# Optimization experiments

Measured on AMD Instinct MI355X. Metric: run time of the kernel, lower is better.

## Reference

```python
import jax, jax.numpy as jnp
from jax import lax
import numpy as np

# (mult_l0, mult_l1, mult_l2) per layer, from CNN.__init__
FEATS = [(5, 0, 0), (10, 3, 0), (10, 3, 1), (16, 8, 1), (16, 8, 1), (16, 8, 1), (1, 0, 0)]
STRIDES = [2, 1, 1, 1, 1, 1]
RELUS = [True, True, True, True, True, False]
SIZE, NRAD, PAD = 7, 3, 3  # SE3Convolution(size=7, n_radial=3, padding=3)


def ch(r):
    return r[0] + 3 * r[1] + 5 * r[2]


def radial_basis():
    # precomputed fixed radial shell basis on the 7^3 kernel grid (stand-in for
    # e3nn's precomputed spherical-harmonic x radial kernel basis)
    r = np.arange(SIZE) - SIZE // 2
    X, Y, Z = np.meshgrid(r, r, r, indexing='ij')
    dist = np.sqrt(X ** 2 + Y ** 2 + Z ** 2)
    centers = np.linspace(0.0, SIZE // 2, NRAD)
    sigma = (SIZE // 2) / (NRAD - 1)
    b = np.exp(-((dist[None] - centers[:, None, None, None]) ** 2) / (2.0 * sigma ** 2))
    return jnp.asarray(b, jnp.float32)  # [NRAD, 7, 7, 7]


def setup_inputs() -> dict:
    key = jax.random.key(0)
    ks = jax.random.split(key, 20)
    inp = {"x": jax.random.normal(ks[0], (2, 5, 32, 32, 32), jnp.float32)}
    for i in range(6):
        cin = ch(FEATS[i]) + 9 * FEATS[i][1]  # after TensorProduct concat
        cout = ch(FEATS[i + 1])
        inp[f"w{i}"] = jax.random.normal(ks[1 + i], (cout, cin, NRAD), jnp.float32) / np.sqrt(cin * SIZE ** 3)
    for i in range(5):
        inp[f"b{i}"] = jax.random.normal(ks[7 + i], (FEATS[i + 1][0],), jnp.float32) * 0.1
    inp["lin_w"] = jax.random.normal(ks[13], (1, 5), jnp.float32)
    inp["lin_b"] = jax.random.normal(ks[14], (1,), jnp.float32)
    inp["alpha"] = jnp.ones((1,), jnp.float32)
    return inp


def _block(x, w, bias, rep_in, rep_out, stride, relu, basis):
    m1, m3, m5 = rep_in
    B = x.shape[0]
    if m3 > 0:
        # TensorProduct on the l=1 fields: self outer product -> 3x3 (9-dim) fields
        sp = x.shape[2:]
        v = x[:, m1:m1 + 3 * m3].reshape(B, m3, 3, *sp)
        t = jnp.einsum('bmixyz,bmjxyz->bmijxyz', v, v).reshape(B, m3 * 9, *sp)
        x = jnp.concatenate([x, t], axis=1)
    # SE3Convolution: learned mixing of precomputed kernel basis, then conv3d
    k = jnp.einsum('oir,rxyz->oixyz', w, basis)  # [Cout, Cin, 7,7,7]
    x = lax.conv_general_dilated(x, k, (stride,) * 3, [(PAD, PAD)] * 3,
                                 dimension_numbers=('NCDHW', 'OIDHW', 'NCDHW'))
    if relu:
        n1, n3, n5 = rep_out
        sp = x.shape[2:]
        # SE3BatchNorm: per-field norm over batch + spatial (per multiplicity channel)
        parts, off = [], 0
        for m, d in ((n1, 1), (n3, 3), (n5, 5)):
            if m == 0:
                continue
            f = x[:, off:off + m * d].reshape(B, m, d, *sp)
            norm2 = jnp.mean(jnp.sum(f * f, axis=2), axis=(0, 2, 3, 4))  # [m]
            f = f / jnp.sqrt(norm2 + 1e-5)[None, :, None, None, None, None]
            parts.append(f.reshape(B, m * d, *sp))
            off += m * d
        x = jnp.concatenate(parts, axis=1)
        # BiasRelu: bias + relu on scalar (l=0) fields only, higher-l pass through
        s = jax.nn.relu(x[:, :n1] + bias[None, :, None, None, None])
        x = jnp.concatenate([s, x[:, n1:]], axis=1)
    return x


def reference(x, w0, w1, w2, w3, w4, w5, b0, b1, b2, b3, b4, lin_w, lin_b, alpha):
    basis = radial_basis()
    ws = [w0, w1, w2, w3, w4, w5]
    bs = [b0, b1, b2, b3, b4, None]
    inp = x
    for i in range(6):
        x = _block(x, ws[i], bs[i], FEATS[i], FEATS[i + 1], STRIDES[i], RELUS[i], basis)
    B = x.shape[0]
    out = x.reshape(B, x.shape[1], -1).mean(-1) * alpha * 0.1  # [B, 1]
    y = inp.reshape(B, 5, -1).sum(-1) @ lin_w.T + lin_b  # [B, 1]
    return out + y
```

## Files before the change

### kernel.cpp

```cpp
#include <hip/hip_runtime.h>
#include <math.h>

static constexpr int OFF_BAS = 0;
static constexpr int OFF_W   = 1280;
static constexpr int OFF_ACC = 37504;
static constexpr int OFF_XA  = 37888;
static constexpr int OFF_XB  = OFF_XA + 761856;
static constexpr int OFF_U   = OFF_XB + 761856;
static constexpr int OFF_Y   = OFF_U + 1105920;

static constexpr int WOFF0 = OFF_W + 0;
static constexpr int WOFF1 = OFF_W + 384;
static constexpr int WOFF2 = OFF_W + 3264;
static constexpr int WOFF3 = OFF_W + 9248;
static constexpr int WOFF4 = OFF_W + 22304;
static constexpr int WOFF5 = OFF_W + 35360;

__device__ __forceinline__ float wred(float s) {
  #pragma unroll
  for (int o = 32; o > 0; o >>= 1) s += __shfl_xor(s, o, 64);
  return s;
}

__global__ __launch_bounds__(128) void prep_kernel(
    const float* __restrict__ w0, const float* __restrict__ w1,
    const float* __restrict__ w2, const float* __restrict__ w3,
    const float* __restrict__ w4, const float* __restrict__ w5,
    float* __restrict__ ws) {
  const int blk = blockIdx.x;
  const int tid = threadIdx.x;
  if (blk == 0) {
    for (int i = tid; i < 1176; i += 128) {
      int tx = i & 7;
      int r  = (i >> 3) % 3;
      int ty = (i / 24) % 7;
      int tz = i / 168;
      float val = 0.f;
      if (tx < 7) {
        double dx = tx - 3, dy = ty - 3, dz = tz - 3;
        double dist = sqrt(dx * dx + dy * dy + dz * dz);
        double d = dist - 1.5 * (double)r;
        val = (float)exp(-(d * d) / 4.5);
      }
      ws[OFF_BAS + i] = val;
    }
    return;
  }
  const int row = blk - 1;
  const int rs[6]    = {0, 24, 96, 232, 368, 504};
  const int kk[6]    = {15, 37, 42, 93, 93, 93};
  const int k4[6]    = {16, 40, 44, 96, 96, 96};
  const int coutt[6] = {19, 24, 45, 45, 45, 1};
  const int cinf[6]  = {5, 46, 51, 117, 117, 117};
  const int chin_[6] = {5, 19, 24, 45, 45, 45};
  const int woff[6]  = {WOFF0, WOFF1, WOFF2, WOFF3, WOFF4, WOFF5};
  const float* wptr[6] = {w0, w1, w2, w3, w4, w5};
  int l = 0;
  while (l < 5 && row >= rs[l + 1]) ++l;
  const int m = row - rs[l];
  const int K = kk[l], K4 = k4[l];
  const float* w = wptr[l];
  float* Wo = ws + woff[l] + m * K4;
  if (l == 0) {
    for (int k = tid; k < 16; k += 128) {
      float v = 0.f;
      if (m < 19 && k < 15) { int c = k / 3, r = k % 3; v = w[(m * 5 + c) * 3 + r]; }
      Wo[k] = v;
    }
    return;
  }
  const int o = m / 3, r = m % 3;
  const int cout = coutt[l];
  const int cf = cinf[l], ch = chin_[l];
  const int itab[6] = {0, 0, 0, 1, 1, 2};
  const int jtab[6] = {0, 1, 2, 1, 2, 2};
  for (int k = tid; k < K4; k += 128) {
    float v = 0.f;
    if (o < cout && k < K) {
      if (k < ch) {
        v = w[(o * cf + k) * 3 + r];
      } else {
        int cc = k - ch;
        int mm = cc / 6, uu = cc % 6;
        int i = itab[uu], j = jtab[uu];
        v = w[(o * cf + ch + mm * 9 + i * 3 + j) * 3 + r];
        if (i != j) v += w[(o * cf + ch + mm * 9 + j * 3 + i) * 3 + r];
      }
    }
    Wo[k] = v;
  }
}

__global__ __launch_bounds__(256) void insum_kernel(const float* __restrict__ x,
                                                    float* __restrict__ insum) {
  const int g = blockIdx.x * 256 + threadIdx.x;
  float4 v = ((const float4*)x)[g];
  float s = v.x + v.y + v.z + v.w;
  s = wred(s);
  if ((threadIdx.x & 63) == 0) atomicAdd(&insum[g >> 13], s);
}

__global__ __launch_bounds__(256) void dw0_kernel(const float* __restrict__ x,
                                                  const float* __restrict__ basg,
                                                  float* __restrict__ z0) {
  const int g = blockIdx.x * 256 + threadIdx.x;
  const int p = g & 4095;
  const int c = (g >> 12) % 5;
  const int b = g / (5 * 4096);
  const int X = p & 15, Y = (p >> 4) & 15, Z = p >> 8;
  const float* xp = x + (((size_t)(b * 5 + c)) << 15);
  float a0 = 0.f, a1 = 0.f, a2 = 0.f;
  for (int tz = 0; tz < 7; ++tz) {
    const int iz = 2 * Z + tz - 3;
    if ((unsigned)iz >= 32u) continue;
    for (int ty = 0; ty < 7; ++ty) {
      const int iy = 2 * Y + ty - 3;
      if ((unsigned)iy >= 32u) continue;
      const float* bb = &basg[(tz * 7 + ty) * 24];
      const float* row = xp + (iz << 10) + (iy << 5);
      #pragma unroll
      for (int tx = 0; tx < 7; ++tx) {
        const int ix = 2 * X + tx - 3;
        float v = ((unsigned)ix < 32u) ? row[ix] : 0.f;
        a0 = fmaf(bb[tx], v, a0);
        a1 = fmaf(bb[8 + tx], v, a1);
        a2 = fmaf(bb[16 + tx], v, a2);
      }
    }
  }
  const size_t base = (((size_t)(b * 15 + c * 3)) << 12) + p;
  z0[base] = a0;
  z0[base + 4096] = a1;
  z0[base + 8192] = a2;
}

template <int K>
__global__ __launch_bounds__(256) void gemm_kernel(
    const float* __restrict__ in, const float* __restrict__ W,
    float* __restrict__ out, int Mreal, float* __restrict__ chsum) {
  constexpr int K4 = (K + 3) & ~3;
  __shared__ float Wl[8 * K4];
  const int b = blockIdx.z;
  const int m0 = blockIdx.y * 8;
  const int p0 = blockIdx.x * 1024 + threadIdx.x * 4;
  for (int i = threadIdx.x; i < 8 * K4; i += 256) Wl[i] = W[m0 * K4 + i];
  __syncthreads();
  const float* ip = in + (((size_t)b * K) << 12) + p0;
  float4 acc[8];
  #pragma unroll
  for (int j = 0; j < 8; ++j) acc[j] = make_float4(0.f, 0.f, 0.f, 0.f);
  int k = 0;
  for (; k + 4 <= K; k += 4) {
    const float4 v0 = *(const float4*)&ip[(size_t)(k + 0) << 12];
    const float4 v1 = *(const float4*)&ip[(size_t)(k + 1) << 12];
    const float4 v2 = *(const float4*)&ip[(size_t)(k + 2) << 12];
    const float4 v3 = *(const float4*)&ip[(size_t)(k + 3) << 12];
    #pragma unroll
    for (int j = 0; j < 8; ++j) {
      const float4 wv = *(const float4*)&Wl[j * K4 + k];
      acc[j].x = fmaf(wv.x, v0.x, acc[j].x); acc[j].y = fmaf(wv.x, v0.y, acc[j].y);
      acc[j].z = fmaf(wv.x, v0.z, acc[j].z); acc[j].w = fmaf(wv.x, v0.w, acc[j].w);
      acc[j].x = fmaf(wv.y, v1.x, acc[j].x); acc[j].y = fmaf(wv.y, v1.y, acc[j].y);
      acc[j].z = fmaf(wv.y, v1.z, acc[j].z); acc[j].w = fmaf(wv.y, v1.w, acc[j].w);
      acc[j].x = fmaf(wv.z, v2.x, acc[j].x); acc[j].y = fmaf(wv.z, v2.y, acc[j].y);
      acc[j].z = fmaf(wv.z, v2.z, acc[j].z); acc[j].w = fmaf(wv.z, v2.w, acc[j].w);
      acc[j].x = fmaf(wv.w, v3.x, acc[j].x); acc[j].y = fmaf(wv.w, v3.y, acc[j].y);
      acc[j].z = fmaf(wv.w, v3.z, acc[j].z); acc[j].w = fmaf(wv.w, v3.w, acc[j].w);
    }
  }
  for (; k < K; ++k) {
    const float4 v = *(const float4*)&ip[(size_t)k << 12];
    #pragma unroll
    for (int j = 0; j < 8; ++j) {
      const float w = Wl[j * K4 + k];
      acc[j].x = fmaf(w, v.x, acc[j].x); acc[j].y = fmaf(w, v.y, acc[j].y);
      acc[j].z = fmaf(w, v.z, acc[j].z); acc[j].w = fmaf(w, v.w, acc[j].w);
    }
  }
  #pragma unroll
  for (int j = 0; j < 8; ++j) {
    const int m = m0 + j;
    if (m < Mreal) *(float4*)&out[(((size_t)(b * Mreal + m)) << 12) + p0] = acc[j];
  }
  if (chsum) {
    #pragma unroll
    for (int j = 0; j < 8; ++j) {
      float s = acc[j].x * acc[j].x + acc[j].y * acc[j].y +
                acc[j].z * acc[j].z + acc[j].w * acc[j].w;
      s = wred(s);
      if ((threadIdx.x & 63) == 0) atomicAdd(&chsum[m0 + j], s);
    }
  }
}

__global__ __launch_bounds__(256) void dwB_kernel(
    const float* __restrict__ u, const float* __restrict__ basg,
    float* __restrict__ y, float* __restrict__ chsum, int cout) {
  __shared__ float lin[15840];
  const int b = blockIdx.y;
  const int o = blockIdx.x >> 2;
  const int zs = blockIdx.x & 3;
  const int tid = threadIdx.x;
  const int z0 = zs * 4;
  const float* ubase = u + (((size_t)(b * 3 * cout + o * 3)) << 12);
  for (int i = tid; i < 15840; i += 256) {
    const int dx = i % 24;
    int t = i / 24;
    const int dy = t % 22;
    t /= 22;
    const int dz = t % 10;
    const int ch = t / 10;
    const int gz = z0 + dz - 3, gy = dy - 3, gx = dx - 4;
    float v = 0.f;
    if ((unsigned)gz < 16u && (unsigned)gy < 16u && (unsigned)gx < 16u)
      v = ubase[(ch << 12) + (gz << 8) + (gy << 4) + gx];
    lin[i] = v;
  }
  __syncthreads();
  const int bx = tid & 3, yy = (tid >> 2) & 15, zz = tid >> 6;
  float acc[4] = {0.f, 0.f, 0.f, 0.f};
  #pragma unroll 1
  for (int tz = 0; tz < 7; ++tz) {
    #pragma unroll 1
    for (int ty = 0; ty < 7; ++ty) {
      const int rb = ((zz + tz) * 22 + (yy + ty)) * 24 + bx * 4;
      float4 a0 = *(const float4*)&lin[rb];
      float4 a1 = *(const float4*)&lin[rb + 4];
      float4 a2 = *(const float4*)&lin[rb + 8];
      float4 b0 = *(const float4*)&lin[rb + 5280];
      float4 b1 = *(const float4*)&lin[rb + 5284];
      float4 b2 = *(const float4*)&lin[rb + 5288];
      float4 c0 = *(const float4*)&lin[rb + 10560];
      float4 c1 = *(const float4*)&lin[rb + 10564];
      float4 c2 = *(const float4*)&lin[rb + 10568];
      const float* bb = &basg[(tz * 7 + ty) * 24];
      const float va[12] = {a0.x,a0.y,a0.z,a0.w,a1.x,a1.y,a1.z,a1.w,a2.x,a2.y,a2.z,a2.w};
      const float vb[12] = {b0.x,b0.y,b0.z,b0.w,b1.x,b1.y,b1.z,b1.w,b2.x,b2.y,b2.z,b2.w};
      const float vc[12] = {c0.x,c0.y,c0.z,c0.w,c1.x,c1.y,c1.z,c1.w,c2.x,c2.y,c2.z,c2.w};
      #pragma unroll
      for (int tx = 0; tx < 7; ++tx) {
        const float w0 = bb[tx], w1 = bb[8 + tx], w2 = bb[16 + tx];
        #pragma unroll
        for (int i2 = 0; i2 < 4; ++i2) {
          acc[i2] = fmaf(w0, va[i2 + tx + 1], acc[i2]);
          acc[i2] = fmaf(w1, vb[i2 + tx + 1], acc[i2]);
          acc[i2] = fmaf(w2, vc[i2 + tx + 1], acc[i2]);
        }
      }
    }
  }
  const int p = ((z0 + zz) << 8) + (yy << 4) + bx * 4;
  float4 outv = {acc[0], acc[1], acc[2], acc[3]};
  *(float4*)&y[(((size_t)(b * cout + o)) << 12) + p] = outv;
  if (chsum) {
    float s = acc[0]*acc[0] + acc[1]*acc[1] + acc[2]*acc[2] + acc[3]*acc[3];
    s = wred(s);
    if ((tid & 63) == 0) atomicAdd(&chsum[o], s);
  }
}

template <int COUT, int N1, int N3>
__global__ __launch_bounds__(64) void post_kernel(
    const float* __restrict__ y, const float* __restrict__ chsum,
    const float* __restrict__ bias, float* __restrict__ xout) {
  constexpr int N5 = (COUT - N1 - 3 * N3) / 5;
  constexpr int CO = COUT + 6 * N3;
  const int b = blockIdx.y;
  const int p = blockIdx.x * 64 + threadIdx.x;
  const float* yp = y + (((size_t)b * COUT) << 12) + p;
  float* xp = xout + (((size_t)b * CO) << 12) + p;
  const float inv = 1.f / 8192.f;
  float vals[COUT];
  #pragma unroll
  for (int c = 0; c < N1; ++c) {
    const float f = 1.f / sqrtf(chsum[c] * inv + 1e-5f);
    const float v = yp[(size_t)c << 12] * f + bias[c];
    vals[c] = v > 0.f ? v : 0.f;
  }
  #pragma unroll
  for (int m = 0; m < N3; ++m) {
    const int c0 = N1 + 3 * m;
    const float f = 1.f / sqrtf((chsum[c0] + chsum[c0 + 1] + chsum[c0 + 2]) * inv + 1e-5f);
    vals[c0]     = yp[(size_t)c0 << 12] * f;
    vals[c0 + 1] = yp[(size_t)(c0 + 1) << 12] * f;
    vals[c0 + 2] = yp[(size_t)(c0 + 2) << 12] * f;
  }
  #pragma unroll
  for (int m = 0; m < N5; ++m) {
    const int c0 = N1 + 3 * N3 + 5 * m;
    const float s5 = chsum[c0] + chsum[c0+1] + chsum[c0+2] + chsum[c0+3] + chsum[c0+4];
    const float f = 1.f / sqrtf(s5 * inv + 1e-5f);
    #pragma unroll
    for (int d = 0; d < 5; ++d) vals[c0 + d] = yp[(size_t)(c0 + d) << 12] * f;
  }
  #pragma unroll
  for (int c = 0; c < COUT; ++c) xp[(size_t)c << 12] = vals[c];
  #pragma unroll
  for (int m = 0; m < N3; ++m) {
    const float v0 = vals[N1 + 3*m], v1 = vals[N1 + 3*m + 1], v2 = vals[N1 + 3*m + 2];
    const float t[6] = {v0*v0, v0*v1, v0*v2, v1*v1, v1*v2, v2*v2};
    #pragma unroll
    for (int uu = 0; uu < 6; ++uu) xp[(size_t)(COUT + m * 6 + uu) << 12] = t[uu];
  }
}

__global__ __launch_bounds__(256) void final_kernel(
    const float* __restrict__ y5, const float* __restrict__ acc,
    const float* __restrict__ lin_w, const float* __restrict__ lin_b,
    const float* __restrict__ alpha, float* __restrict__ out) {
  const int b = blockIdx.x;
  const int tid = threadIdx.x;
  float s = 0.f;
  for (int i = tid; i < 4096; i += 256) s += y5[(b << 12) + i];
  s = wred(s);
  __shared__ float ls[4];
  if ((tid & 63) == 0) ls[tid >> 6] = s;
  __syncthreads();
  if (tid == 0) {
    const float t = ls[0] + ls[1] + ls[2] + ls[3];
    float res = t * (1.f / 4096.f) * alpha[0] * 0.1f;
    const float* insum = acc + 240;
    for (int c = 0; c < 5; ++c) res += insum[b * 5 + c] * lin_w[c];
    res += lin_b[0];
    out[b] = res;
  }
}

extern "C" void kernel_launch(void* const* d_in, const int* in_sizes, int n_in,
                              void* d_out, int out_size, void* d_ws, size_t ws_size,
                              hipStream_t stream) {
  const float* x  = (const float*)d_in[0];
  const float* w0 = (const float*)d_in[1];
  const float* w1 = (const float*)d_in[2];
  const float* w2 = (const float*)d_in[3];
  const float* w3 = (const float*)d_in[4];
  const float* w4 = (const float*)d_in[5];
  const float* w5 = (const float*)d_in[6];
  const float* b0 = (const float*)d_in[7];
  const float* b1 = (const float*)d_in[8];
  const float* b2 = (const float*)d_in[9];
  const float* b3 = (const float*)d_in[10];
  const float* b4 = (const float*)d_in[11];
  const float* lw = (const float*)d_in[12];
  const float* lb = (const float*)d_in[13];
  const float* al = (const float*)d_in[14];
  float* out = (float*)d_out;
  float* ws = (float*)d_ws;

  float* bas = ws + OFF_BAS;
  float* acc = ws + OFF_ACC;
  float* XA = ws + OFF_XA;
  float* XB = ws + OFF_XB;
  float* U  = ws + OFF_U;
  float* Y  = ws + OFF_Y;

  hipMemsetAsync(acc, 0, 256 * sizeof(float), stream);
  hipLaunchKernelGGL(prep_kernel, dim3(513), dim3(128), 0, stream, w0, w1, w2, w3, w4, w5, ws);
  hipLaunchKernelGGL(insum_kernel, dim3(320), dim3(256), 0, stream, x, acc + 240);

  hipLaunchKernelGGL(dw0_kernel, dim3(160), dim3(256), 0, stream, x, bas, U);
  hipLaunchKernelGGL(gemm_kernel<15>, dim3(4, 3, 2), dim3(256), 0, stream,
                     U, ws + WOFF0, Y, 19, acc);
  hipLaunchKernelGGL((post_kernel<19, 10, 3>), dim3(64, 2), dim3(64), 0, stream, Y, acc, b0, XA);

  hipLaunchKernelGGL(gemm_kernel<37>, dim3(4, 9, 2), dim3(256), 0, stream,
                     XA, ws + WOFF1, U, 72, (float*)nullptr);
  hipLaunchKernelGGL(dwB_kernel, dim3(96, 2), dim3(256), 0, stream, U, bas, Y, acc + 48, 24);
  hipLaunchKernelGGL((post_kernel<24, 10, 3>), dim3(64, 2), dim3(64), 0, stream, Y, acc + 48, b1, XB);

  hipLaunchKernelGGL(gemm_kernel<42>, dim3(4, 17, 2), dim3(256), 0, stream,
                     XB, ws + WOFF2, U, 135, (float*)nullptr);
  hipLaunchKernelGGL(dwB_kernel, dim3(180, 2), dim3(256), 0, stream, U, bas, Y, acc + 96, 45);
  hipLaunchKernelGGL((post_kernel<45, 16, 8>), dim3(64, 2), dim3(64), 0, stream, Y, acc + 96, b2, XA);

  hipLaunchKernelGGL(gemm_kernel<93>, dim3(4, 17, 2), dim3(256), 0, stream,
                     XA, ws + WOFF3, U, 135, (float*)nullptr);
  hipLaunchKernelGGL(dwB_kernel, dim3(180, 2), dim3(256), 0, stream, U, bas, Y, acc + 144, 45);
  hipLaunchKernelGGL((post_kernel<45, 16, 8>), dim3(64, 2), dim3(64), 0, stream, Y, acc + 144, b3, XB);

  hipLaunchKernelGGL(gemm_kernel<93>, dim3(4, 17, 2), dim3(256), 0, stream,
                     XB, ws + WOFF4, U, 135, (float*)nullptr);
  hipLaunchKernelGGL(dwB_kernel, dim3(180, 2), dim3(256), 0, stream, U, bas, Y, acc + 192, 45);
  hipLaunchKernelGGL((post_kernel<45, 16, 8>), dim3(64, 2), dim3(64), 0, stream, Y, acc + 192, b4, XA);

  hipLaunchKernelGGL(gemm_kernel<93>, dim3(4, 1, 2), dim3(256), 0, stream,
                     XA, ws + WOFF5, U, 3, (float*)nullptr);
  hipLaunchKernelGGL(dwB_kernel, dim3(4, 2), dim3(256), 0, stream, U, bas, Y, (float*)nullptr, 1);

  hipLaunchKernelGGL(final_kernel, dim3(2), dim3(256), 0, stream, Y, acc, lw, lb, al, out);
}
```

Before: 530.0 us.

## Split depthwise conv tiles in y, use float4 swizzled LDS staging

The depthwise 7^3 conv kernel now tiles output as 4z x 8y x 16x per block with 128 threads instead of 4z x 16y x 16x with 256 threads, doubling the grid. The halo is loaded with float4 global reads into 32-float rows with an XOR swizzle on odd rows to cut LDS bank conflicts. The smaller per-block LDS footprint should let more blocks share a CU, improving occupancy and load balance. The cost is a larger y-halo overhead (14 staged rows for 8 outputs instead of 22 for 16) and extra index arithmetic.

```diff
diff --git a/kernel.cpp b/kernel.cpp
--- a/kernel.cpp
+++ b/kernel.cpp
@@ -193,46 +193,53 @@
   }
 }
 
-__global__ __launch_bounds__(256) void dwB_kernel(
+__global__ __launch_bounds__(128) void dwB_kernel(
     const float* __restrict__ u, const float* __restrict__ basg,
     float* __restrict__ y, float* __restrict__ chsum, int cout) {
-  __shared__ float lin[15840];
+  __shared__ float lin[13440];
   const int b = blockIdx.y;
-  const int o = blockIdx.x >> 2;
-  const int zs = blockIdx.x & 3;
+  const int o = blockIdx.x >> 3;
+  const int rem = blockIdx.x & 7;
+  const int zs = rem >> 1, yh = rem & 1;
+  const int z0 = zs * 4, y0 = yh * 8;
   const int tid = threadIdx.x;
-  const int z0 = zs * 4;
   const float* ubase = u + (((size_t)(b * 3 * cout + o * 3)) << 12);
-  for (int i = tid; i < 15840; i += 256) {
-    const int dx = i % 24;
-    int t = i / 24;
-    const int dy = t % 22;
-    t /= 22;
-    const int dz = t % 10;
-    const int ch = t / 10;
-    const int gz = z0 + dz - 3, gy = dy - 3, gx = dx - 4;
-    float v = 0.f;
-    if ((unsigned)gz < 16u && (unsigned)gy < 16u && (unsigned)gx < 16u)
-      v = ubase[(ch << 12) + (gz << 8) + (gy << 4) + gx];
-    lin[i] = v;
+  for (int i = tid; i < 3360; i += 128) {
+    const int g = i & 7;
+    const int row = i >> 3;
+    const int ch = row / 140;
+    const int rr = row - ch * 140;
+    const int dz = rr / 14;
+    const int dy = rr - dz * 14;
+    const int gz = z0 + dz - 3, gy = y0 + dy - 3;
+    float4 v = make_float4(0.f, 0.f, 0.f, 0.f);
+    if (g >= 1 && g <= 4 && (unsigned)gz < 16u && (unsigned)gy < 16u)
+      v = *(const float4*)&ubase[(ch << 12) + (gz << 8) + (gy << 4) + ((g - 1) << 2)];
+    const int sw = (dy & 1) << 2;
+    *(float4*)&lin[row * 32 + ((g ^ sw) << 2)] = v;
   }
   __syncthreads();
-  const int bx = tid & 3, yy = (tid >> 2) & 15, zz = tid >> 6;
+  const int bx = tid & 3, yy = (tid >> 2) & 7, zz = tid >> 5;
   float acc[4] = {0.f, 0.f, 0.f, 0.f};
   #pragma unroll 1
   for (int tz = 0; tz < 7; ++tz) {
     #pragma unroll 1
     for (int ty = 0; ty < 7; ++ty) {
-      const int rb = ((zz + tz) * 22 + (yy + ty)) * 24 + bx * 4;
-      float4 a0 = *(const float4*)&lin[rb];
-      float4 a1 = *(const float4*)&lin[rb + 4];
-      float4 a2 = *(const float4*)&lin[rb + 8];
-      float4 b0 = *(const float4*)&lin[rb + 5280];
-      float4 b1 = *(const float4*)&lin[rb + 5284];
-      float4 b2 = *(const float4*)&lin[rb + 5288];
-      float4 c0 = *(const float4*)&lin[rb + 10560];
-      float4 c1 = *(const float4*)&lin[rb + 10564];
-      float4 c2 = *(const float4*)&lin[rb + 10568];
+      const int dy = yy + ty;
+      const int sw = (dy & 1) << 2;
+      const int r0 = ((zz + tz) * 14 + dy) * 32;
+      const int i0 = r0 + (((bx + 0) ^ sw) << 2);
+      const int i1 = r0 + (((bx + 1) ^ sw) << 2);
+      const int i2w = r0 + (((bx + 2) ^ sw) << 2);
+      float4 a0 = *(const float4*)&lin[i0];
+      float4 a1 = *(const float4*)&lin[i1];
+      float4 a2 = *(const float4*)&lin[i2w];
+      float4 b0 = *(const float4*)&lin[i0 + 4480];
+      float4 b1 = *(const float4*)&lin[i1 + 4480];
+      float4 b2 = *(const float4*)&lin[i2w + 4480];
+      float4 c0 = *(const float4*)&lin[i0 + 8960];
+      float4 c1 = *(const float4*)&lin[i1 + 8960];
+      float4 c2 = *(const float4*)&lin[i2w + 8960];
       const float* bb = &basg[(tz * 7 + ty) * 24];
       const float va[12] = {a0.x,a0.y,a0.z,a0.w,a1.x,a1.y,a1.z,a1.w,a2.x,a2.y,a2.z,a2.w};
       const float vb[12] = {b0.x,b0.y,b0.z,b0.w,b1.x,b1.y,b1.z,b1.w,b2.x,b2.y,b2.z,b2.w};
@@ -249,7 +256,7 @@
       }
     }
   }
-  const int p = ((z0 + zz) << 8) + (yy << 4) + bx * 4;
+  const int p = ((z0 + zz) << 8) + ((y0 + yy) << 4) + bx * 4;
   float4 outv = {acc[0], acc[1], acc[2], acc[3]};
   *(float4*)&y[(((size_t)(b * cout + o)) << 12) + p] = outv;
   if (chsum) {
@@ -365,27 +372,27 @@
 
   hipLaunchKernelGGL(gemm_kernel<37>, dim3(4, 9, 2), dim3(256), 0, stream,
                      XA, ws + WOFF1, U, 72, (float*)nullptr);
-  hipLaunchKernelGGL(dwB_kernel, dim3(96, 2), dim3(256), 0, stream, U, bas, Y, acc + 48, 24);
+  hipLaunchKernelGGL(dwB_kernel, dim3(192, 2), dim3(128), 0, stream, U, bas, Y, acc + 48, 24);
   hipLaunchKernelGGL((post_kernel<24, 10, 3>), dim3(64, 2), dim3(64), 0, stream, Y, acc + 48, b1, XB);
 
   hipLaunchKernelGGL(gemm_kernel<42>, dim3(4, 17, 2), dim3(256), 0, stream,
                      XB, ws + WOFF2, U, 135, (float*)nullptr);
-  hipLaunchKernelGGL(dwB_kernel, dim3(180, 2), dim3(256), 0, stream, U, bas, Y, acc + 96, 45);
+  hipLaunchKernelGGL(dwB_kernel, dim3(360, 2), dim3(128), 0, stream, U, bas, Y, acc + 96, 45);
   hipLaunchKernelGGL((post_kernel<45, 16, 8>), dim3(64, 2), dim3(64), 0, stream, Y, acc + 96, b2, XA);
 
   hipLaunchKernelGGL(gemm_kernel<93>, dim3(4, 17, 2), dim3(256), 0, stream,
                      XA, ws + WOFF3, U, 135, (float*)nullptr);
-  hipLaunchKernelGGL(dwB_kernel, dim3(180, 2), dim3(256), 0, stream, U, bas, Y, acc + 144, 45);
+  hipLaunchKernelGGL(dwB_kernel, dim3(360, 2), dim3(128), 0, stream, U, bas, Y, acc + 144, 45);
   hipLaunchKernelGGL((post_kernel<45, 16, 8>), dim3(64, 2), dim3(64), 0, stream, Y, acc + 144, b3, XB);
 
   hipLaunchKernelGGL(gemm_kernel<93>, dim3(4, 17, 2), dim3(256), 0, stream,
                      XB, ws + WOFF4, U, 135, (float*)nullptr);
-  hipLaunchKernelGGL(dwB_kernel, dim3(180, 2), dim3(256), 0, stream, U, bas, Y, acc + 192, 45);
+  hipLaunchKernelGGL(dwB_kernel, dim3(360, 2), dim3(128), 0, stream, U, bas, Y, acc + 192, 45);
   hipLaunchKernelGGL((post_kernel<45, 16, 8>), dim3(64, 2), dim3(64), 0, stream, Y, acc + 192, b4, XA);
 
   hipLaunchKernelGGL(gemm_kernel<93>, dim3(4, 1, 2), dim3(256), 0, stream,
                      XA, ws + WOFF5, U, 3, (float*)nullptr);
-  hipLaunchKernelGGL(dwB_kernel, dim3(4, 2), dim3(256), 0, stream, U, bas, Y, (float*)nullptr, 1);
+  hipLaunchKernelGGL(dwB_kernel, dim3(8, 2), dim3(128), 0, stream, U, bas, Y, (float*)nullptr, 1);
 
   hipLaunchKernelGGL(final_kernel, dim3(2), dim3(256), 0, stream, Y, acc, lw, lb, al, out);
 }
```

Result: faster. 443.1 us (-16.4%).

## Drop LDS staging in depthwise conv; each thread computes full 16-wide x row

Applied to the files above, without the earlier changes.

The depthwise 7^3 conv kernel no longer stages a padded halo tile in shared memory. Each 64-thread block has every thread load whole 16-float rows straight from global memory and accumulate a full output x-row in registers, so x-direction reuse happens in registers. This removes the shared-memory fill, its index arithmetic and the barrier. In exchange, reuse across neighbouring y/z rows now depends on the cache, and there are 4x fewer threads per block, which can lower occupancy and latency hiding.

```diff
diff --git a/kernel.cpp b/kernel.cpp
--- a/kernel.cpp
+++ b/kernel.cpp
@@ -193,69 +193,65 @@
   }
 }
 
-__global__ __launch_bounds__(256) void dwB_kernel(
+__global__ __launch_bounds__(64) void dwB_kernel(
     const float* __restrict__ u, const float* __restrict__ basg,
     float* __restrict__ y, float* __restrict__ chsum, int cout) {
-  __shared__ float lin[15840];
   const int b = blockIdx.y;
   const int o = blockIdx.x >> 2;
   const int zs = blockIdx.x & 3;
   const int tid = threadIdx.x;
-  const int z0 = zs * 4;
-  const float* ubase = u + (((size_t)(b * 3 * cout + o * 3)) << 12);
-  for (int i = tid; i < 15840; i += 256) {
-    const int dx = i % 24;
-    int t = i / 24;
-    const int dy = t % 22;
-    t /= 22;
-    const int dz = t % 10;
-    const int ch = t / 10;
-    const int gz = z0 + dz - 3, gy = dy - 3, gx = dx - 4;
-    float v = 0.f;
-    if ((unsigned)gz < 16u && (unsigned)gy < 16u && (unsigned)gx < 16u)
-      v = ubase[(ch << 12) + (gz << 8) + (gy << 4) + gx];
-    lin[i] = v;
-  }
-  __syncthreads();
-  const int bx = tid & 3, yy = (tid >> 2) & 15, zz = tid >> 6;
-  float acc[4] = {0.f, 0.f, 0.f, 0.f};
+  const int yy = tid & 15, zz = tid >> 4;
+  const int Z = zs * 4 + zz;
+  const float* ub = u + (((size_t)(b * 3 * cout + o * 3)) << 12);
+  float acc[16];
+  #pragma unroll
+  for (int i = 0; i < 16; ++i) acc[i] = 0.f;
   #pragma unroll 1
   for (int tz = 0; tz < 7; ++tz) {
+    const int gz = Z + tz - 3;
+    const bool zok = (unsigned)gz < 16u;
     #pragma unroll 1
     for (int ty = 0; ty < 7; ++ty) {
-      const int rb = ((zz + tz) * 22 + (yy + ty)) * 24 + bx * 4;
-      float4 a0 = *(const float4*)&lin[rb];
-      float4 a1 = *(const float4*)&lin[rb + 4];
-      float4 a2 = *(const float4*)&lin[rb + 8];
-      float4 b0 = *(const float4*)&lin[rb + 5280];
-      float4 b1 = *(const float4*)&lin[rb + 5284];
-      float4 b2 = *(const float4*)&lin[rb + 5288];
-      float4 c0 = *(const float4*)&lin[rb + 10560];
-      float4 c1 = *(const float4*)&lin[rb + 10564];
-      float4 c2 = *(const float4*)&lin[rb + 10568];
+      const int gy = yy + ty - 3;
+      const bool ok = zok && ((unsigned)gy < 16u);
+      const float* rp = ub + (gz << 8) + (gy << 4);
+      float4 A[3][4];
+      #pragma unroll
+      for (int ch = 0; ch < 3; ++ch) {
+        #pragma unroll
+        for (int q = 0; q < 4; ++q) {
+          A[ch][q] = ok ? *(const float4*)(rp + (ch << 12) + (q << 2))
+                        : make_float4(0.f, 0.f, 0.f, 0.f);
+        }
+      }
       const float* bb = &basg[(tz * 7 + ty) * 24];
-      const float va[12] = {a0.x,a0.y,a0.z,a0.w,a1.x,a1.y,a1.z,a1.w,a2.x,a2.y,a2.z,a2.w};
-      const float vb[12] = {b0.x,b0.y,b0.z,b0.w,b1.x,b1.y,b1.z,b1.w,b2.x,b2.y,b2.z,b2.w};
-      const float vc[12] = {c0.x,c0.y,c0.z,c0.w,c1.x,c1.y,c1.z,c1.w,c2.x,c2.y,c2.z,c2.w};
       #pragma unroll
-      for (int tx = 0; tx < 7; ++tx) {
-        const float w0 = bb[tx], w1 = bb[8 + tx], w2 = bb[16 + tx];
+      for (int ch = 0; ch < 3; ++ch) {
         #pragma unroll
-        for (int i2 = 0; i2 < 4; ++i2) {
-          acc[i2] = fmaf(w0, va[i2 + tx + 1], acc[i2]);
-          acc[i2] = fmaf(w1, vb[i2 + tx + 1], acc[i2]);
-          acc[i2] = fmaf(w2, vc[i2 + tx + 1], acc[i2]);
+        for (int tx = 0; tx < 7; ++tx) {
+          const float w = bb[ch * 8 + tx];
+          #pragma unroll
+          for (int x = 0; x < 16; ++x) {
+            const int j = x + tx - 3;
+            if (j >= 0 && j < 16)
+              acc[x] = fmaf(w, ((const float*)&A[ch][j >> 2])[j & 3], acc[x]);
+          }
         }
       }
     }
   }
-  const int p = ((z0 + zz) << 8) + (yy << 4) + bx * 4;
-  float4 outv = {acc[0], acc[1], acc[2], acc[3]};
-  *(float4*)&y[(((size_t)(b * cout + o)) << 12) + p] = outv;
+  float* yp = y + (((size_t)(b * cout + o)) << 12) + (Z << 8) + (yy << 4);
+  #pragma unroll
+  for (int q = 0; q < 4; ++q) {
+    float4 outv = {acc[4*q], acc[4*q+1], acc[4*q+2], acc[4*q+3]};
+    *(float4*)(yp + 4 * q) = outv;
+  }
   if (chsum) {
-    float s = acc[0]*acc[0] + acc[1]*acc[1] + acc[2]*acc[2] + acc[3]*acc[3];
+    float s = 0.f;
+    #pragma unroll
+    for (int x = 0; x < 16; ++x) s += acc[x] * acc[x];
     s = wred(s);
-    if ((tid & 63) == 0) atomicAdd(&chsum[o], s);
+    if (tid == 0) atomicAdd(&chsum[o], s);
   }
 }
 
@@ -365,27 +361,27 @@
 
   hipLaunchKernelGGL(gemm_kernel<37>, dim3(4, 9, 2), dim3(256), 0, stream,
                      XA, ws + WOFF1, U, 72, (float*)nullptr);
-  hipLaunchKernelGGL(dwB_kernel, dim3(96, 2), dim3(256), 0, stream, U, bas, Y, acc + 48, 24);
+  hipLaunchKernelGGL(dwB_kernel, dim3(96, 2), dim3(64), 0, stream, U, bas, Y, acc + 48, 24);
   hipLaunchKernelGGL((post_kernel<24, 10, 3>), dim3(64, 2), dim3(64), 0, stream, Y, acc + 48, b1, XB);
 
   hipLaunchKernelGGL(gemm_kernel<42>, dim3(4, 17, 2), dim3(256), 0, stream,
                      XB, ws + WOFF2, U, 135, (float*)nullptr);
-  hipLaunchKernelGGL(dwB_kernel, dim3(180, 2), dim3(256), 0, stream, U, bas, Y, acc + 96, 45);
+  hipLaunchKernelGGL(dwB_kernel, dim3(180, 2), dim3(64), 0, stream, U, bas, Y, acc + 96, 45);
   hipLaunchKernelGGL((post_kernel<45, 16, 8>), dim3(64, 2), dim3(64), 0, stream, Y, acc + 96, b2, XA);
 
   hipLaunchKernelGGL(gemm_kernel<93>, dim3(4, 17, 2), dim3(256), 0, stream,
                      XA, ws + WOFF3, U, 135, (float*)nullptr);
-  hipLaunchKernelGGL(dwB_kernel, dim3(180, 2), dim3(256), 0, stream, U, bas, Y, acc + 144, 45);
+  hipLaunchKernelGGL(dwB_kernel, dim3(180, 2), dim3(64), 0, stream, U, bas, Y, acc + 144, 45);
   hipLaunchKernelGGL((post_kernel<45, 16, 8>), dim3(64, 2), dim3(64), 0, stream, Y, acc + 144, b3, XB);
 
   hipLaunchKernelGGL(gemm_kernel<93>, dim3(4, 17, 2), dim3(256), 0, stream,
                      XB, ws + WOFF4, U, 135, (float*)nullptr);
-  hipLaunchKernelGGL(dwB_kernel, dim3(180, 2), dim3(256), 0, stream, U, bas, Y, acc + 192, 45);
+  hipLaunchKernelGGL(dwB_kernel, dim3(180, 2), dim3(64), 0, stream, U, bas, Y, acc + 192, 45);
   hipLaunchKernelGGL((post_kernel<45, 16, 8>), dim3(64, 2), dim3(64), 0, stream, Y, acc + 192, b4, XA);
 
   hipLaunchKernelGGL(gemm_kernel<93>, dim3(4, 1, 2), dim3(256), 0, stream,
                      XA, ws + WOFF5, U, 3, (float*)nullptr);
-  hipLaunchKernelGGL(dwB_kernel, dim3(4, 2), dim3(256), 0, stream, U, bas, Y, (float*)nullptr, 1);
+  hipLaunchKernelGGL(dwB_kernel, dim3(4, 2), dim3(64), 0, stream, U, bas, Y, (float*)nullptr, 1);
 
   hipLaunchKernelGGL(final_kernel, dim3(2), dim3(256), 0, stream, Y, acc, lw, lb, al, out);
 }
```

Measured after the change: 715.9 us. +35.1%, slower.
